# Kernel tuning notes

Hardware: AMD Instinct MI355X
Metric: run time of the kernel (lower is better)

Reference implementation:

```python
import jax, jax.numpy as jnp
import numpy as np

B, NQ, D, NH, L, P = 8, 1000, 256, 8, 4, 4
DFF = 1024
HD = D // NH
SHAPES = np.array([[128, 128], [64, 64], [32, 32], [16, 16]], dtype=np.int64)
S = int((SHAPES[:, 0] * SHAPES[:, 1]).sum())  # 21760
LEVEL_START = np.concatenate([np.zeros(1, np.int64), np.cumsum(SHAPES[:, 0] * SHAPES[:, 1])[:-1]])


def setup_inputs() -> dict:
    key = jax.random.key(0)
    ks = jax.random.split(key, 20)
    w = lambda k, shape, s=0.02: jax.random.normal(k, shape, jnp.float32) * s
    z = lambda n: jnp.zeros((n,), jnp.float32)
    return dict(
        query=w(ks[0], (B, NQ, D), 1.0),
        query_pos=w(ks[1], (B, NQ, D), 1.0),
        reference_points=jax.random.uniform(ks[2], (B, NQ, L, 4), jnp.float32),
        input_flatten=w(ks[3], (B, S, D), 1.0),
        input_spatial_shapes=SHAPES,
        input_level_start_index=LEVEL_START,
        Wq=w(ks[4], (D, D)), bq=z(D), Wk=w(ks[5], (D, D)), bk=z(D),
        Wv=w(ks[6], (D, D)), bv=z(D), Wo=w(ks[7], (D, D)), bo=z(D),
        ln1_g=jnp.ones((D,), jnp.float32), ln1_b=z(D),
        W_off=w(ks[8], (D, NH * L * P * 2)), b_off=z(NH * L * P * 2),
        W_attn=w(ks[9], (D, NH * L * P)), b_attn=z(NH * L * P),
        W_val=w(ks[10], (D, D)), b_val=z(D),
        W_cout=w(ks[11], (D, D)), b_cout=z(D),
        ln2_g=jnp.ones((D,), jnp.float32), ln2_b=z(D),
        W1=w(ks[12], (D, DFF)), b1=z(DFF),
        W2=w(ks[13], (DFF, D)), b2=z(D),
        ln3_g=jnp.ones((D,), jnp.float32), ln3_b=z(D),
    )


def layer_norm(x, g, b, eps=1e-5):
    mu = x.mean(-1, keepdims=True)
    var = ((x - mu) ** 2).mean(-1, keepdims=True)
    return (x - mu) / jnp.sqrt(var + eps) * g + b


def _ms_deform(value, shapes_np, loc, aw):
    # value: (B,S,NH,HD); loc: (B,Nq,NH,L,P,2) in [0,1]; aw: (B,Nq,NH,L,P)
    Bz, _, nh, hd = value.shape
    Nq = loc.shape[1]
    awt = aw.transpose(0, 2, 1, 3, 4)  # (B,NH,Nq,L,P)
    acc = jnp.zeros((Bz, nh, Nq, hd), value.dtype)
    start = 0
    for lvl in range(shapes_np.shape[0]):
        Hl, Wl = int(shapes_np[lvl, 0]), int(shapes_np[lvl, 1])
        vf = value[:, start:start + Hl * Wl].transpose(0, 2, 1, 3)  # (B,NH,Hl*Wl,HD)
        start += Hl * Wl
        # grid_sample align_corners=False: pixel coord = loc * size - 0.5
        lx = loc[:, :, :, lvl, :, 0].transpose(0, 2, 1, 3) * Wl - 0.5  # (B,NH,Nq,P)
        ly = loc[:, :, :, lvl, :, 1].transpose(0, 2, 1, 3) * Hl - 0.5
        x0 = jnp.floor(lx); y0 = jnp.floor(ly)
        tx = lx - x0; ty = ly - y0
        x0i = x0.astype(jnp.int32); y0i = y0.astype(jnp.int32)

        def gather(xi, yi):
            valid = (xi >= 0) & (xi < Wl) & (yi >= 0) & (yi < Hl)
            idx = jnp.clip(yi, 0, Hl - 1) * Wl + jnp.clip(xi, 0, Wl - 1)
            out = jnp.take_along_axis(vf, idx.reshape(Bz, nh, Nq * P)[..., None], axis=2)
            return out.reshape(Bz, nh, Nq, P, hd) * valid[..., None]

        g00 = gather(x0i, y0i)
        g01 = gather(x0i + 1, y0i)
        g10 = gather(x0i, y0i + 1)
        g11 = gather(x0i + 1, y0i + 1)
        samp = (g00 * ((1 - tx) * (1 - ty))[..., None] + g01 * (tx * (1 - ty))[..., None]
                + g10 * ((1 - tx) * ty)[..., None] + g11 * (tx * ty)[..., None])  # (B,NH,Nq,P,HD)
        acc = acc + jnp.einsum('bhqp,bhqpd->bhqd', awt[:, :, :, lvl], samp)
    return acc.transpose(0, 2, 1, 3).reshape(Bz, Nq, nh * hd)


def reference(query, query_pos, reference_points, input_flatten, input_spatial_shapes,
              input_level_start_index, Wq, bq, Wk, bk, Wv, bv, Wo, bo, ln1_g, ln1_b,
              W_off, b_off, W_attn, b_attn, W_val, b_val, W_cout, b_cout, ln2_g, ln2_b,
              W1, b1, W2, b2, ln3_g, ln3_b):
    Bz, Nq, Dm = query.shape
    # --- self-attention (post-norm), pos added to Q/K only ---
    qp = query + query_pos
    q = (qp @ Wq + bq).reshape(Bz, Nq, NH, HD)
    k = (qp @ Wk + bk).reshape(Bz, Nq, NH, HD)
    v = (query @ Wv + bv).reshape(Bz, Nq, NH, HD)
    att = jax.nn.softmax(jnp.einsum('bqhd,bkhd->bhqk', q, k) / jnp.sqrt(jnp.float32(HD)), axis=-1)
    sa = jnp.einsum('bhqk,bkhd->bqhd', att, v).reshape(Bz, Nq, Dm) @ Wo + bo
    x = layer_norm(query + sa, ln1_g, ln1_b)
    # --- deformable cross-attention ---
    q2 = x + query_pos
    value = (input_flatten @ W_val + b_val).reshape(Bz, -1, NH, HD)
    off = (q2 @ W_off + b_off).reshape(Bz, Nq, NH, L, P, 2)
    aw = jax.nn.softmax((q2 @ W_attn + b_attn).reshape(Bz, Nq, NH, L * P), axis=-1)
    aw = aw.reshape(Bz, Nq, NH, L, P)
    rp = reference_points  # (B,Nq,L,4) cxcywh
    loc = rp[:, :, None, :, None, :2] + off / P * rp[:, :, None, :, None, 2:] * 0.5
    shapes_np = np.asarray(input_spatial_shapes)
    ca = _ms_deform(value, shapes_np, loc, aw) @ W_cout + b_cout
    x = layer_norm(x + ca, ln2_g, ln2_b)
    # --- FFN ---
    ffn = jax.nn.relu(x @ W1 + b1) @ W2 + b2
    return layer_norm(x + ffn, ln3_g, ln3_b)
```

## Files before the change

kernel.cpp:

```cpp
#include <hip/hip_runtime.h>
#include <hip/hip_bf16.h>

#define B_   8
#define NQ_  1000
#define D_   256
#define NH_  8
#define L_   4
#define P_   4
#define DFF_ 1024
#define HD_  32
#define S_   21760
#define NTOK (B_*NQ_)

typedef short  bf16x8 __attribute__((ext_vector_type(8)));
typedef float  f32x4  __attribute__((ext_vector_type(4)));

#define WAITBAR(N) asm volatile("s_waitcnt vmcnt(" #N ") lgkmcnt(0)\n\ts_barrier" ::: "memory")
#define ENDBAR()   asm volatile("s_barrier" ::: "memory")

__device__ inline unsigned short f32_to_bf16_bits(float f) {
    unsigned int u = __float_as_uint(f);
    unsigned int rounding = 0x7FFFu + ((u >> 16) & 1u);
    u += rounding;
    return (unsigned short)(u >> 16);
}
__device__ inline float bf16_bits_to_f32(unsigned short b) {
    return __uint_as_float(((unsigned int)b) << 16);
}
__device__ inline unsigned int pack_trunc(float f0, float f1) {
    return __builtin_amdgcn_perm(__float_as_uint(f1), __float_as_uint(f0), 0x07060302u);
}
__device__ inline void async_copy16(const void* g, void* l) {
    __builtin_amdgcn_global_load_lds((const __attribute__((address_space(1))) unsigned int*)g,
                                     (__attribute__((address_space(3))) unsigned int*)l, 16, 0, 0);
}

struct PrepArgs {
    const float* wsrc[10];
    unsigned short* wdst[10];
    int wK[10], wN[10];
    const float* bq; const float* bk; const float* boff; const float* battn;
    float* qkb; float* oab;
    const float* query; const float* qpos;
    unsigned short* q_bf; unsigned short* qp_bf;
};
__global__ __launch_bounds__(256) void prep_k(PrepArgs P)
{
    const int bid = blockIdx.x, tid = threadIdx.x;
    if (bid < 640) {
        const int job = bid >> 6, tile = bid & 63;
        const int K = P.wK[job], N = P.wN[job];
        const int tilesN = N >> 6;
        if (tile >= (K >> 6) * tilesN) return;
        const int kt = tile / tilesN, nt = tile - kt * tilesN;
        const int k0 = kt * 64, n0 = nt * 64;
        __shared__ unsigned short t_[64][65];
        const float* src = P.wsrc[job];
        unsigned short* dst = P.wdst[job];
        const int cc = tid & 63, rr = tid >> 6;
        #pragma unroll
        for (int i = 0; i < 16; i++) {
            int k = i * 4 + rr;
            t_[k][cc] = f32_to_bf16_bits(src[(size_t)(k0 + k) * N + n0 + cc]);
        }
        __syncthreads();
        #pragma unroll
        for (int i = 0; i < 16; i++) {
            int n = i * 4 + rr;
            dst[(size_t)(n0 + n) * K + k0 + cc] = t_[cc][n];
        }
    } else if (bid == 640) {
        P.qkb[tid]       = P.bq[tid];
        P.qkb[256 + tid] = P.bk[tid];
        P.oab[tid]       = P.boff[tid];
        if (tid < 128) P.oab[256 + tid] = P.battn[tid];
    } else {
        const int base = (bid - 641) * 1024 + tid;
        float4 fq[4][2], fp[4][2];
        #pragma unroll
        for (int i = 0; i < 4; i++) {
            const float* q = P.query + (size_t)(base + i * 256) * 8;
            const float* p = P.qpos  + (size_t)(base + i * 256) * 8;
            fq[i][0] = *reinterpret_cast<const float4*>(q);
            fq[i][1] = *reinterpret_cast<const float4*>(q + 4);
            fp[i][0] = *reinterpret_cast<const float4*>(p);
            fp[i][1] = *reinterpret_cast<const float4*>(p + 4);
        }
        #pragma unroll
        for (int i = 0; i < 4; i++) {
            uint4 tq, tp;
            tq.x = pack_trunc(fq[i][0].x, fq[i][0].y);
            tq.y = pack_trunc(fq[i][0].z, fq[i][0].w);
            tq.z = pack_trunc(fq[i][1].x, fq[i][1].y);
            tq.w = pack_trunc(fq[i][1].z, fq[i][1].w);
            tp.x = pack_trunc(fq[i][0].x + fp[i][0].x, fq[i][0].y + fp[i][0].y);
            tp.y = pack_trunc(fq[i][0].z + fp[i][0].z, fq[i][0].w + fp[i][0].w);
            tp.z = pack_trunc(fq[i][1].x + fp[i][1].x, fq[i][1].y + fp[i][1].y);
            tp.w = pack_trunc(fq[i][1].z + fp[i][1].z, fq[i][1].w + fp[i][1].w);
            *reinterpret_cast<uint4*>(P.q_bf  + (size_t)(base + i * 256) * 8) = tq;
            *reinterpret_cast<uint4*>(P.qp_bf + (size_t)(base + i * 256) * 8) = tp;
        }
    }
}

__global__ __launch_bounds__(256) void vgemmF(const float* __restrict__ Af,
                                              const unsigned short* __restrict__ Bt,
                                              const float* __restrict__ bias,
                                              unsigned short* __restrict__ Cb)
{
    constexpr int K = 256;
    constexpr int N = 256;
    __shared__ __align__(16) float          sA[2][128 * 32];
    __shared__ __align__(16) unsigned short sB[2][128 * 32];
    const int tid = threadIdx.x;
    const int w = tid >> 6, l = tid & 63;
    const int n0 = blockIdx.x * 128, m0 = blockIdx.y * 128;
    const int wr = w >> 1, wc = w & 1;
    const int lq = l & 15, g = l >> 4;

    f32x4 acc[4][4];
    #pragma unroll
    for (int i = 0; i < 4; i++)
        #pragma unroll
        for (int j = 0; j < 4; j++)
            #pragma unroll
            for (int r = 0; r < 4; r++) acc[i][j][r] = 0.f;

    auto issueA = [&](int t, int buf) {
        #pragma unroll
        for (int r = 0; r < 4; r++) {
            int lin = (r * 256 + tid) * 16;
            int row = lin >> 7;
            int kb  = (lin & 127) ^ ((row & 3) << 5);
            async_copy16(Af + (size_t)(m0 + row) * K + t * 32 + (kb >> 2),
                         (char*)sA[buf] + lin);
        }
    };
    auto issueB = [&](int t, int buf) {
        #pragma unroll
        for (int r = 0; r < 2; r++) {
            int lin = (r * 256 + tid) * 16;
            int row = lin >> 6;
            int kb  = (lin & 63) ^ ((row & 3) << 4);
            async_copy16(Bt + (size_t)(n0 + row) * K + t * 32 + (kb >> 1),
                         (char*)sB[buf] + lin);
        }
    };

    issueA(0, 0);
    issueB(0, 0);

    for (int t = 0; t < 8; t++) {
        const int cur = t & 1;
        if (t + 1 < 8) {
            issueA(t + 1, cur ^ 1);
            issueB(t + 1, cur ^ 1);
            WAITBAR(6);
        } else {
            WAITBAR(0);
        }

        bf16x8 afr[4], bfr[4];
        #pragma unroll
        for (int mi = 0; mi < 4; mi++) {
            int row = wr * 64 + mi * 16 + lq;
            int off = (g * 32) ^ ((row & 3) << 5);
            const char* p = (const char*)sA[cur] + row * 128 + off;
            float4 a0 = *reinterpret_cast<const float4*>(p);
            float4 a1 = *reinterpret_cast<const float4*>(p + 16);
            uint4 u;
            u.x = pack_trunc(a0.x, a0.y);
            u.y = pack_trunc(a0.z, a0.w);
            u.z = pack_trunc(a1.x, a1.y);
            u.w = pack_trunc(a1.z, a1.w);
            afr[mi] = *reinterpret_cast<bf16x8*>(&u);
        }
        #pragma unroll
        for (int ni = 0; ni < 4; ni++) {
            int row = wc * 64 + ni * 16 + lq;
            int off = (g * 16) ^ ((row & 3) << 4);
            bfr[ni] = *reinterpret_cast<const bf16x8*>((const char*)sB[cur] + row * 64 + off);
        }
        #pragma unroll
        for (int mi = 0; mi < 4; mi++)
            #pragma unroll
            for (int ni = 0; ni < 4; ni++)
                acc[mi][ni] = __builtin_amdgcn_mfma_f32_16x16x32_bf16(
                    afr[mi], bfr[ni], acc[mi][ni], 0, 0, 0);
        ENDBAR();
    }

    #pragma unroll
    for (int mi = 0; mi < 4; mi++) {
        #pragma unroll
        for (int ni = 0; ni < 4; ni++) {
            int col = n0 + wc * 64 + ni * 16 + lq;
            float bz = bias[col];
            #pragma unroll
            for (int rg = 0; rg < 4; rg++) {
                int row = m0 + wr * 64 + mi * 16 + g * 4 + rg;
                Cb[(size_t)row * N + col] = f32_to_bf16_bits(acc[mi][ni][rg] + bz);
            }
        }
    }
}

template<bool RELU, int CMODE, int BN, int K>
__global__ __launch_bounds__(256) void bgemm(const unsigned short* __restrict__ Ab,
                                             const unsigned short* __restrict__ Bt,
                                             const float* __restrict__ bias,
                                             float* __restrict__ Cf,
                                             unsigned short* __restrict__ Cb,
                                             int N)
{
    constexpr int NF   = BN / 16;
    constexpr int KF   = K / 32;
    constexpr int ROWB = K * 2;
    constexpr int FILL = BN * ROWB / 4096;

    __shared__ __align__(16) unsigned short sB[BN * K];

    const int tid = threadIdx.x;
    const int w = tid >> 6, l = tid & 63;
    const int g = l >> 4, lr = l & 15;
    const int n0 = blockIdx.x * BN;

    #pragma unroll
    for (int r = 0; r < FILL; r++) {
        int lin = (r * 256 + tid) * 16;
        int row = lin / ROWB;
        int kb  = (lin & (ROWB - 1)) ^ ((row & 7) << 4);
        async_copy16(Bt + (size_t)(n0 + row) * K + (kb >> 1), (char*)sB + lin);
    }
    asm volatile("s_waitcnt vmcnt(0)\n\ts_barrier" ::: "memory");

    float bz[NF];
    #pragma unroll
    for (int nf = 0; nf < NF; nf++) bz[nf] = bias[n0 + nf * 16 + lr];

    const int m0w = blockIdx.y * 64 + w * 16;
    const int arow = m0w + lr;

    f32x4 acc[NF];
    #pragma unroll
    for (int nf = 0; nf < NF; nf++)
        #pragma unroll
        for (int r = 0; r < 4; r++) acc[nf][r] = 0.f;

    #pragma unroll
    for (int kf = 0; kf < KF; kf++) {
        bf16x8 af = *reinterpret_cast<const bf16x8*>(Ab + (size_t)arow * K + kf * 32 + g * 8);
        #pragma unroll
        for (int nf = 0; nf < NF; nf++) {
            int brow = nf * 16 + lr;
            bf16x8 bf = *reinterpret_cast<const bf16x8*>(
                (const char*)sB + brow * ROWB + ((kf * 64 + g * 16) ^ ((brow & 7) << 4)));
            acc[nf] = __builtin_amdgcn_mfma_f32_16x16x32_bf16(af, bf, acc[nf], 0, 0, 0);
        }
    }

    #pragma unroll
    for (int nf = 0; nf < NF; nf++) {
        int col = n0 + nf * 16 + lr;
        if constexpr (CMODE == 2) {
            int row0 = m0w + g * 4;
            int bb = row0 / 1000;
            int key = row0 - bb * 1000;
            ushort4 q4;
            q4.x = f32_to_bf16_bits(acc[nf][0] + bz[nf]);
            q4.y = f32_to_bf16_bits(acc[nf][1] + bz[nf]);
            q4.z = f32_to_bf16_bits(acc[nf][2] + bz[nf]);
            q4.w = f32_to_bf16_bits(acc[nf][3] + bz[nf]);
            *reinterpret_cast<ushort4*>(Cb + (size_t)bb * 262144 + (size_t)col * 1024 + key) = q4;
        } else {
            #pragma unroll
            for (int rg = 0; rg < 4; rg++) {
                int row = m0w + g * 4 + rg;
                float v = acc[nf][rg] + bz[nf];
                if (RELU) v = fmaxf(v, 0.f);
                if constexpr (CMODE == 1)
                    Cb[(size_t)row * N + col] = f32_to_bf16_bits(v);
                else
                    Cf[(size_t)row * N + col] = v;
            }
        }
    }
}

__global__ __launch_bounds__(256) void fattn_k(const unsigned short* __restrict__ qk,
                                               const unsigned short* __restrict__ vt,
                                               unsigned short* __restrict__ sa)
{
    const int b = blockIdx.z, h = blockIdx.y;
    const int tid = threadIdx.x;
    const int w = tid >> 6, l = tid & 63;
    const int lq = l & 15, g = l >> 4;
    const int q0 = blockIdx.x * 64 + w * 16;

    __shared__ __align__(16) unsigned short Ks[2][128 * 32];
    __shared__ __align__(16) unsigned short Vs[2][32 * 128];
    __shared__ __align__(16) unsigned short Ps[4][16 * 128];

    int qrow = q0 + lq; if (qrow > NQ_ - 1) qrow = NQ_ - 1;
    const bf16x8 qfrag = *reinterpret_cast<const bf16x8*>(
        qk + ((size_t)(b * NQ_ + qrow)) * 512 + h * 32 + g * 8);

    f32x4 O0 = {0.f, 0.f, 0.f, 0.f}, O1 = {0.f, 0.f, 0.f, 0.f};
    float m = -1e30f, lsum = 0.f;
    const float scale = 0.17677669529663687f;

    const size_t kbase = (size_t)b * (NQ_ * 512) + 256 + h * 32;
    const size_t vbase = (size_t)b * 262144 + (size_t)(h * 32) * 1024;
    const int swz = (lq & 7) << 4;

    auto issueKV = [&](int kt, int buf) {
        #pragma unroll
        for (int r = 0; r < 2; r++) {
            int lin = (r * 256 + tid) * 16;
            int krow = lin >> 6;
            int kb = (lin & 63) ^ ((krow & 7) << 4);
            async_copy16(qk + kbase + (size_t)(kt * 128 + krow) * 512 + (kb >> 1),
                         (char*)Ks[buf] + lin);
            int d = lin >> 8;
            int vb = (lin & 255) ^ ((d & 7) << 4);
            async_copy16(vt + vbase + (size_t)d * 1024 + kt * 128 + (vb >> 1),
                         (char*)Vs[buf] + lin);
        }
    };

    issueKV(0, 0);

    for (int kt = 0; kt < 8; kt++) {
        const int k0 = kt * 128;
        const int cur = kt & 1;
        asm volatile("s_waitcnt vmcnt(0) lgkmcnt(0)\n\ts_barrier" ::: "memory");
        if (kt < 7) issueKV(kt + 1, cur ^ 1);

        const unsigned short* Kc = Ks[cur];
        const unsigned short* Vc = Vs[cur];

        float t[8][4];
        float tmax = -1e30f;
        const bool tail = (k0 + 128 > NQ_);
        #pragma unroll
        for (int ni = 0; ni < 8; ni++) {
            int row = ni * 16 + lq;
            bf16x8 kf = *reinterpret_cast<const bf16x8*>(
                (const char*)Kc + row * 64 + ((g * 16) ^ swz));
            f32x4 st = __builtin_amdgcn_mfma_f32_16x16x32_bf16(
                kf, qfrag, (f32x4){0.f, 0.f, 0.f, 0.f}, 0, 0, 0);
            #pragma unroll
            for (int rg = 0; rg < 4; rg++) {
                float tv = st[rg] * scale;
                if (tail) {
                    int key = k0 + ni * 16 + g * 4 + rg;
                    tv = (key < NQ_) ? tv : -1e30f;
                }
                t[ni][rg] = tv;
                tmax = fmaxf(tmax, tv);
            }
        }
        tmax = fmaxf(tmax, __shfl_xor(tmax, 16));
        tmax = fmaxf(tmax, __shfl_xor(tmax, 32));
        float mnew = fmaxf(m, tmax);
        float corr = __expf(m - mnew);
        m = mnew;

        float rs = 0.f;
        unsigned int pk[8][2];
        #pragma unroll
        for (int ni = 0; ni < 8; ni++) {
            float p0 = __expf(t[ni][0] - mnew);
            float p1 = __expf(t[ni][1] - mnew);
            float p2 = __expf(t[ni][2] - mnew);
            float p3 = __expf(t[ni][3] - mnew);
            rs += (p0 + p1) + (p2 + p3);
            pk[ni][0] = ((unsigned)f32_to_bf16_bits(p0)) | (((unsigned)f32_to_bf16_bits(p1)) << 16);
            pk[ni][1] = ((unsigned)f32_to_bf16_bits(p2)) | (((unsigned)f32_to_bf16_bits(p3)) << 16);
        }
        rs += __shfl_xor(rs, 16);
        rs += __shfl_xor(rs, 32);
        lsum = lsum * corr + rs;

        float c0 = __shfl(corr, g * 4 + 0);
        float c1 = __shfl(corr, g * 4 + 1);
        float c2 = __shfl(corr, g * 4 + 2);
        float c3 = __shfl(corr, g * 4 + 3);
        O0[0] *= c0; O0[1] *= c1; O0[2] *= c2; O0[3] *= c3;
        O1[0] *= c0; O1[1] *= c1; O1[2] *= c2; O1[3] *= c3;

        unsigned short* Pw = Ps[w];
        #pragma unroll
        for (int ni = 0; ni < 8; ni++) {
            int byteoff = lq * 256 + ((ni * 32 + g * 8) ^ swz);
            *reinterpret_cast<uint2*>((char*)Pw + byteoff) = make_uint2(pk[ni][0], pk[ni][1]);
        }

        #pragma unroll
        for (int c = 0; c < 4; c++) {
            int rb = (c * 64 + g * 16) ^ swz;
            bf16x8 pa = *reinterpret_cast<const bf16x8*>((const char*)Pw + lq * 256 + rb);
            bf16x8 v0 = *reinterpret_cast<const bf16x8*>((const char*)Vc + lq * 256 + rb);
            bf16x8 v1 = *reinterpret_cast<const bf16x8*>((const char*)Vc + (16 + lq) * 256 + rb);
            O0 = __builtin_amdgcn_mfma_f32_16x16x32_bf16(pa, v0, O0, 0, 0, 0);
            O1 = __builtin_amdgcn_mfma_f32_16x16x32_bf16(pa, v1, O1, 0, 0, 0);
        }
    }

    float linv = 1.f / lsum;
    float i0 = __shfl(linv, g * 4 + 0);
    float i1 = __shfl(linv, g * 4 + 1);
    float i2 = __shfl(linv, g * 4 + 2);
    float i3 = __shfl(linv, g * 4 + 3);
    float iv[4] = {i0, i1, i2, i3};
    #pragma unroll
    for (int rg = 0; rg < 4; rg++) {
        int qg = q0 + g * 4 + rg;
        if (qg < NQ_) {
            size_t obase = ((size_t)(b * NQ_ + qg)) * 256 + h * 32;
            sa[obase + lq]      = f32_to_bf16_bits(O0[rg] * iv[rg]);
            sa[obase + 16 + lq] = f32_to_bf16_bits(O1[rg] * iv[rg]);
        }
    }
}

template<int OM>
__global__ __launch_bounds__(256) void ln_k(const float* __restrict__ a,
                                            const float* __restrict__ bsum,
                                            const float* __restrict__ pos,
                                            const float* __restrict__ g,
                                            const float* __restrict__ be,
                                            float* __restrict__ out,
                                            unsigned short* __restrict__ outb)
{
    const int wave = threadIdx.x >> 6, lane = threadIdx.x & 63;
    const int row = blockIdx.x * 4 + wave;
    float4 xa = reinterpret_cast<const float4*>(a + (size_t)row * 256)[lane];
    float4 xb = reinterpret_cast<const float4*>(bsum + (size_t)row * 256)[lane];
    float4 x = {xa.x + xb.x, xa.y + xb.y, xa.z + xb.z, xa.w + xb.w};
    float s  = x.x + x.y + x.z + x.w;
    float ss = x.x * x.x + x.y * x.y + x.z * x.z + x.w * x.w;
    #pragma unroll
    for (int off = 32; off > 0; off >>= 1) {
        s  += __shfl_xor(s, off);
        ss += __shfl_xor(ss, off);
    }
    float mu  = s * (1.f / 256.f);
    float var = ss * (1.f / 256.f) - mu * mu;
    float rstd = rsqrtf(var + 1e-5f);
    float4 gv = reinterpret_cast<const float4*>(g)[lane];
    float4 bv = reinterpret_cast<const float4*>(be)[lane];
    float4 o = {(x.x - mu) * rstd * gv.x + bv.x,
                (x.y - mu) * rstd * gv.y + bv.y,
                (x.z - mu) * rstd * gv.z + bv.z,
                (x.w - mu) * rstd * gv.w + bv.w};
    reinterpret_cast<float4*>(out + (size_t)row * 256)[lane] = o;
    if constexpr (OM == 1) {
        ushort4 q4;
        q4.x = f32_to_bf16_bits(o.x); q4.y = f32_to_bf16_bits(o.y);
        q4.z = f32_to_bf16_bits(o.z); q4.w = f32_to_bf16_bits(o.w);
        *reinterpret_cast<ushort4*>(outb + (size_t)row * 256 + lane * 4) = q4;
    } else if constexpr (OM == 2) {
        float4 pv = reinterpret_cast<const float4*>(pos + (size_t)row * 256)[lane];
        ushort4 q4;
        q4.x = f32_to_bf16_bits(o.x + pv.x); q4.y = f32_to_bf16_bits(o.y + pv.y);
        q4.z = f32_to_bf16_bits(o.z + pv.z); q4.w = f32_to_bf16_bits(o.w + pv.w);
        *reinterpret_cast<ushort4*>(outb + (size_t)row * 256 + lane * 4) = q4;
    }
}

__device__ inline unsigned int samp2(const unsigned short* __restrict__ v,
                                     int b, int st, int Wl, int Hl,
                                     int x, int y, int hc)
{
    bool valid = (x >= 0) & (x < Wl) & (y >= 0) & (y < Hl);
    int xc = min(max(x, 0), Wl - 1);
    int yc = min(max(y, 0), Hl - 1);
    size_t idx = ((size_t)(b * S_ + st + yc * Wl + xc)) * 256 + hc;
    unsigned int val = *reinterpret_cast<const unsigned int*>(v + idx);
    return valid ? val : 0u;
}

__global__ __launch_bounds__(256) void deform_k(const float* __restrict__ rp,
                                                const float* __restrict__ oa,
                                                const unsigned short* __restrict__ value,
                                                unsigned short* __restrict__ ca)
{
    const int tk = threadIdx.x >> 7;
    const int tok = blockIdx.x * 2 + tk;
    const int b = tok / NQ_;
    const int h = (threadIdx.x >> 4) & 7;
    const int cp = threadIdx.x & 15;
    const int hc = h * 32 + cp * 2;

    const float* awp = oa + (size_t)tok * 384 + 256 + h * 16;
    float w[16];
    float mx = -1e30f;
    #pragma unroll
    for (int i = 0; i < 16; i++) { w[i] = awp[i]; mx = fmaxf(mx, w[i]); }
    float sum = 0.f;
    #pragma unroll
    for (int i = 0; i < 16; i++) { w[i] = __expf(w[i] - mx); sum += w[i]; }
    const float inv = 1.f / sum;

    const float* rpp  = rp + (size_t)tok * (L_ * 4);
    const float* offp = oa + (size_t)tok * 384 + h * 32;

    const int lvlW[4] = {128, 64, 32, 16};
    const int lvlS[4] = {0, 16384, 20480, 21504};

    float acc0 = 0.f, acc1 = 0.f;
    #pragma unroll
    for (int l = 0; l < 4; l++) {
        const int Wl = lvlW[l], Hl = lvlW[l], st = lvlS[l];
        const float cx = rpp[l * 4 + 0], cy = rpp[l * 4 + 1];
        const float cw = rpp[l * 4 + 2], chh = rpp[l * 4 + 3];
        #pragma unroll
        for (int p = 0; p < 4; p++) {
            float ox = offp[l * 8 + p * 2 + 0];
            float oy = offp[l * 8 + p * 2 + 1];
            float lx = (cx + ox * 0.25f * cw * 0.5f) * Wl - 0.5f;
            float ly = (cy + oy * 0.25f * chh * 0.5f) * Hl - 0.5f;
            float x0f = floorf(lx), y0f = floorf(ly);
            float tx = lx - x0f, ty = ly - y0f;
            int x0 = (int)x0f, y0 = (int)y0f;
            unsigned int u00 = samp2(value, b, st, Wl, Hl, x0,     y0,     hc);
            unsigned int u01 = samp2(value, b, st, Wl, Hl, x0 + 1, y0,     hc);
            unsigned int u10 = samp2(value, b, st, Wl, Hl, x0,     y0 + 1, hc);
            unsigned int u11 = samp2(value, b, st, Wl, Hl, x0 + 1, y0 + 1, hc);
            float w00 = (1.f - tx) * (1.f - ty), w01 = tx * (1.f - ty);
            float w10 = (1.f - tx) * ty,         w11 = tx * ty;
            float g0 = bf16_bits_to_f32((unsigned short)u00) * w00
                     + bf16_bits_to_f32((unsigned short)u01) * w01
                     + bf16_bits_to_f32((unsigned short)u10) * w10
                     + bf16_bits_to_f32((unsigned short)u11) * w11;
            float g1 = bf16_bits_to_f32((unsigned short)(u00 >> 16)) * w00
                     + bf16_bits_to_f32((unsigned short)(u01 >> 16)) * w01
                     + bf16_bits_to_f32((unsigned short)(u10 >> 16)) * w10
                     + bf16_bits_to_f32((unsigned short)(u11 >> 16)) * w11;
            float wa = w[l * 4 + p] * inv;
            acc0 += wa * g0;
            acc1 += wa * g1;
        }
    }
    unsigned int packed = ((unsigned)f32_to_bf16_bits(acc0)) | (((unsigned)f32_to_bf16_bits(acc1)) << 16);
    *reinterpret_cast<unsigned int*>(ca + (size_t)tok * 256 + hc) = packed;
}

extern "C" void kernel_launch(void* const* d_in, const int* in_sizes, int n_in,
                              void* d_out, int out_size, void* d_ws, size_t ws_size,
                              hipStream_t stream)
{
    const float* query      = (const float*)d_in[0];
    const float* query_pos  = (const float*)d_in[1];
    const float* ref_pts    = (const float*)d_in[2];
    const float* input_flat = (const float*)d_in[3];
    const float* Wq = (const float*)d_in[6];  const float* bq = (const float*)d_in[7];
    const float* Wk = (const float*)d_in[8];  const float* bk = (const float*)d_in[9];
    const float* Wv = (const float*)d_in[10]; const float* bv = (const float*)d_in[11];
    const float* Wo = (const float*)d_in[12]; const float* bo = (const float*)d_in[13];
    const float* ln1g = (const float*)d_in[14]; const float* ln1b = (const float*)d_in[15];
    const float* W_off = (const float*)d_in[16]; const float* b_off = (const float*)d_in[17];
    const float* W_attn = (const float*)d_in[18]; const float* b_attn = (const float*)d_in[19];
    const float* W_val = (const float*)d_in[20]; const float* b_val = (const float*)d_in[21];
    const float* W_cout = (const float*)d_in[22]; const float* b_cout = (const float*)d_in[23];
    const float* ln2g = (const float*)d_in[24]; const float* ln2b = (const float*)d_in[25];
    const float* W1 = (const float*)d_in[26]; const float* b1 = (const float*)d_in[27];
    const float* W2 = (const float*)d_in[28]; const float* b2 = (const float*)d_in[29];
    const float* ln3g = (const float*)d_in[30]; const float* ln3b = (const float*)d_in[31];
    float* out = (float*)d_out;

    char* base = (char*)d_ws;
    size_t off = 0;
    auto alloc = [&](size_t bytes) { void* p = base + off; off += (bytes + 255) & ~(size_t)255; return p; };
    unsigned short* value_bf = (unsigned short*)alloc((size_t)B_ * S_ * 256 * 2);
    unsigned short* qk_bf = (unsigned short*)alloc((size_t)NTOK * 1024 * 2);
    unsigned short* h_bf = qk_bf;
    unsigned short* vt = (unsigned short*)alloc((size_t)B_ * 256 * 1024 * 2);
    float* oa_buf = (float*)alloc((size_t)NTOK * 384 * 4);
    float* tmp0   = (float*)alloc((size_t)NTOK * 256 * 4);
    float* x1     = (float*)alloc((size_t)NTOK * 256 * 4);
    float* x2     = (float*)alloc((size_t)NTOK * 256 * 4);
    unsigned short* sc_bf  = (unsigned short*)alloc((size_t)NTOK * 256 * 2);
    unsigned short* q_bf   = (unsigned short*)alloc((size_t)NTOK * 256 * 2);
    unsigned short* qp_bf  = (unsigned short*)alloc((size_t)NTOK * 256 * 2);
    unsigned short* x1p_bf = (unsigned short*)alloc((size_t)NTOK * 256 * 2);
    unsigned short* x2_bf  = (unsigned short*)alloc((size_t)NTOK * 256 * 2);
    unsigned short* wqk   = (unsigned short*)alloc(512 * 256 * 2);
    unsigned short* wv    = (unsigned short*)alloc(256 * 256 * 2);
    unsigned short* wo    = (unsigned short*)alloc(256 * 256 * 2);
    unsigned short* woa   = (unsigned short*)alloc(384 * 256 * 2);
    unsigned short* wval  = (unsigned short*)alloc(256 * 256 * 2);
    unsigned short* wcout = (unsigned short*)alloc(256 * 256 * 2);
    unsigned short* w1t   = (unsigned short*)alloc(1024 * 256 * 2);
    unsigned short* w2t   = (unsigned short*)alloc(256 * 1024 * 2);
    float* qkbias = (float*)alloc(512 * 4);
    float* oabias = (float*)alloc(384 * 4);

    dim3 blk(256);

    PrepArgs P;
    P.wsrc[0] = Wq;    P.wdst[0] = wqk;               P.wK[0] = 256;  P.wN[0] = 256;
    P.wsrc[1] = Wk;    P.wdst[1] = wqk + 256 * 256;   P.wK[1] = 256;  P.wN[1] = 256;
    P.wsrc[2] = Wv;    P.wdst[2] = wv;                P.wK[2] = 256;  P.wN[2] = 256;
    P.wsrc[3] = Wo;    P.wdst[3] = wo;                P.wK[3] = 256;  P.wN[3] = 256;
    P.wsrc[4] = W_off; P.wdst[4] = woa;               P.wK[4] = 256;  P.wN[4] = 256;
    P.wsrc[5] = W_attn;P.wdst[5] = woa + 256 * 256;   P.wK[5] = 256;  P.wN[5] = 128;
    P.wsrc[6] = W_val; P.wdst[6] = wval;              P.wK[6] = 256;  P.wN[6] = 256;
    P.wsrc[7] = W_cout;P.wdst[7] = wcout;             P.wK[7] = 256;  P.wN[7] = 256;
    P.wsrc[8] = W1;    P.wdst[8] = w1t;               P.wK[8] = 256;  P.wN[8] = 1024;
    P.wsrc[9] = W2;    P.wdst[9] = w2t;               P.wK[9] = 1024; P.wN[9] = 256;
    P.bq = bq; P.bk = bk; P.boff = b_off; P.battn = b_attn;
    P.qkb = qkbias; P.oab = oabias;
    P.query = query; P.qpos = query_pos; P.q_bf = q_bf; P.qp_bf = qp_bf;
    prep_k<<<891, blk, 0, stream>>>(P);

    bgemm<false, 1,  64, 256><<<dim3(8, 125), blk, 0, stream>>>(qp_bf, wqk, qkbias, nullptr, qk_bf, 512);
    bgemm<false, 2,  64, 256><<<dim3(4, 125), blk, 0, stream>>>(q_bf,  wv,  bv,     nullptr, vt,    256);
    fattn_k<<<dim3(16, NH_, B_), blk, 0, stream>>>(qk_bf, vt, sc_bf);
    bgemm<false, 0,  64, 256><<<dim3(4, 125), blk, 0, stream>>>(sc_bf, wo, bo, tmp0, nullptr, 256);
    ln_k<2><<<NTOK / 4, blk, 0, stream>>>(query, tmp0, query_pos, ln1g, ln1b, x1, x1p_bf);

    vgemmF<<<dim3(2, 1360), blk, 0, stream>>>(input_flat, wval, b_val, value_bf);
    bgemm<false, 0,  64, 256><<<dim3(6, 125), blk, 0, stream>>>(x1p_bf, woa, oabias, oa_buf, nullptr, 384);
    deform_k<<<NTOK / 2, blk, 0, stream>>>(ref_pts, oa_buf, value_bf, sc_bf);
    bgemm<false, 0,  64, 256><<<dim3(4, 125), blk, 0, stream>>>(sc_bf, wcout, b_cout, tmp0, nullptr, 256);
    ln_k<1><<<NTOK / 4, blk, 0, stream>>>(x1, tmp0, nullptr, ln2g, ln2b, x2, x2_bf);

    bgemm<true,  1,  64, 256><<<dim3(16, 125), blk, 0, stream>>>(x2_bf, w1t, b1, nullptr, h_bf, 1024);
    bgemm<false, 0,  32, 1024><<<dim3(8, 125), blk, 0, stream>>>(h_bf, w2t, b2, tmp0, nullptr, 256);
    ln_k<0><<<NTOK / 4, blk, 0, stream>>>(x2, tmp0, nullptr, ln3g, ln3b, out, nullptr);
}
```

Baseline: 253.7 us.

## Register-prefetch value GEMM with bf16 LDS tiles and 4-buffer ring

The value-projection GEMM stops using async global-to-LDS copies of fp32 A tiles. Each thread now loads A and B into registers three K-steps ahead, converts A to bf16 before writing it to swizzled LDS, and cycles through a 4-deep LDS ring so only one barrier per step is needed. This halves LDS traffic and footprint for A, removes the per-fragment conversion from the MFMA loop, and drops the trailing barrier. The cost is higher register pressure from 18 float4 prefetch registers per thread and reliance on the ring depth to avoid write-after-read hazards.

```diff
diff --git a/kernel.cpp b/kernel.cpp
--- a/kernel.cpp
+++ b/kernel.cpp
@@ -16,7 +16,7 @@
 typedef float  f32x4  __attribute__((ext_vector_type(4)));
 
 #define WAITBAR(N) asm volatile("s_waitcnt vmcnt(" #N ") lgkmcnt(0)\n\ts_barrier" ::: "memory")
-#define ENDBAR()   asm volatile("s_barrier" ::: "memory")
+#define LBAR()     asm volatile("s_waitcnt lgkmcnt(0)\n\ts_barrier" ::: "memory")
 
 __device__ inline unsigned short f32_to_bf16_bits(float f) {
     unsigned int u = __float_as_uint(f);
@@ -103,21 +103,57 @@
     }
 }
 
-__global__ __launch_bounds__(256) void vgemmF(const float* __restrict__ Af,
+__global__ __launch_bounds__(256) void vgemmP(const float* __restrict__ Af,
                                               const unsigned short* __restrict__ Bt,
                                               const float* __restrict__ bias,
                                               unsigned short* __restrict__ Cb)
 {
     constexpr int K = 256;
     constexpr int N = 256;
-    __shared__ __align__(16) float          sA[2][128 * 32];
-    __shared__ __align__(16) unsigned short sB[2][128 * 32];
+    __shared__ __align__(16) unsigned short sA[4][128 * 32];
+    __shared__ __align__(16) unsigned short sB[4][128 * 32];
+
     const int tid = threadIdx.x;
     const int w = tid >> 6, l = tid & 63;
     const int n0 = blockIdx.x * 128, m0 = blockIdx.y * 128;
     const int wr = w >> 1, wc = w & 1;
     const int lq = l & 15, g = l >> 4;
 
+    const int ldr = tid >> 1;
+    const int ldh = tid & 1;
+    const float*          aSrc = Af + (size_t)(m0 + ldr) * K + ldh * 16;
+    const unsigned short* bSrc = Bt + (size_t)(n0 + ldr) * K + ldh * 16;
+    const int wswz = ((ldr & 3) << 4);
+    const int o0 = (ldh * 32)      ^ wswz;
+    const int o1 = (ldh * 32 + 16) ^ wswz;
+
+    float4 fA[3][4];
+    float4 fB[3][2];
+
+    auto loadStage = [&](int t, int s) {
+        const float4* ap = reinterpret_cast<const float4*>(aSrc + t * 32);
+        fA[s][0] = ap[0]; fA[s][1] = ap[1]; fA[s][2] = ap[2]; fA[s][3] = ap[3];
+        const float4* bp = reinterpret_cast<const float4*>(bSrc + t * 32);
+        fB[s][0] = bp[0]; fB[s][1] = bp[1];
+    };
+    auto writeStage = [&](int s, int buf) {
+        uint4 c0, c1;
+        c0.x = pack_trunc(fA[s][0].x, fA[s][0].y);
+        c0.y = pack_trunc(fA[s][0].z, fA[s][0].w);
+        c0.z = pack_trunc(fA[s][1].x, fA[s][1].y);
+        c0.w = pack_trunc(fA[s][1].z, fA[s][1].w);
+        c1.x = pack_trunc(fA[s][2].x, fA[s][2].y);
+        c1.y = pack_trunc(fA[s][2].z, fA[s][2].w);
+        c1.z = pack_trunc(fA[s][3].x, fA[s][3].y);
+        c1.w = pack_trunc(fA[s][3].z, fA[s][3].w);
+        char* abase = (char*)sA[buf] + ldr * 64;
+        *reinterpret_cast<uint4*>(abase + o0) = c0;
+        *reinterpret_cast<uint4*>(abase + o1) = c1;
+        char* bbase = (char*)sB[buf] + ldr * 64;
+        *reinterpret_cast<float4*>(bbase + o0) = fB[s][0];
+        *reinterpret_cast<float4*>(bbase + o1) = fB[s][1];
+    };
+
     f32x4 acc[4][4];
     #pragma unroll
     for (int i = 0; i < 4; i++)
@@ -126,60 +162,30 @@
             #pragma unroll
             for (int r = 0; r < 4; r++) acc[i][j][r] = 0.f;
 
-    auto issueA = [&](int t, int buf) {
-        #pragma unroll
-        for (int r = 0; r < 4; r++) {
-            int lin = (r * 256 + tid) * 16;
-            int row = lin >> 7;
-            int kb  = (lin & 127) ^ ((row & 3) << 5);
-            async_copy16(Af + (size_t)(m0 + row) * K + t * 32 + (kb >> 2),
-                         (char*)sA[buf] + lin);
-        }
-    };
-    auto issueB = [&](int t, int buf) {
-        #pragma unroll
-        for (int r = 0; r < 2; r++) {
-            int lin = (r * 256 + tid) * 16;
-            int row = lin >> 6;
-            int kb  = (lin & 63) ^ ((row & 3) << 4);
-            async_copy16(Bt + (size_t)(n0 + row) * K + t * 32 + (kb >> 1),
-                         (char*)sB[buf] + lin);
-        }
-    };
-
-    issueA(0, 0);
-    issueB(0, 0);
-
+    loadStage(0, 0);
+    loadStage(1, 1);
+    loadStage(2, 2);
+
+    #pragma unroll
     for (int t = 0; t < 8; t++) {
-        const int cur = t & 1;
-        if (t + 1 < 8) {
-            issueA(t + 1, cur ^ 1);
-            issueB(t + 1, cur ^ 1);
-            WAITBAR(6);
-        } else {
-            WAITBAR(0);
-        }
+        const int s   = t % 3;
+        const int buf = t & 3;
+        writeStage(s, buf);
+        if (t + 3 < 8) loadStage(t + 3, s);
+        LBAR();
 
         bf16x8 afr[4], bfr[4];
         #pragma unroll
         for (int mi = 0; mi < 4; mi++) {
             int row = wr * 64 + mi * 16 + lq;
-            int off = (g * 32) ^ ((row & 3) << 5);
-            const char* p = (const char*)sA[cur] + row * 128 + off;
-            float4 a0 = *reinterpret_cast<const float4*>(p);
-            float4 a1 = *reinterpret_cast<const float4*>(p + 16);
-            uint4 u;
-            u.x = pack_trunc(a0.x, a0.y);
-            u.y = pack_trunc(a0.z, a0.w);
-            u.z = pack_trunc(a1.x, a1.y);
-            u.w = pack_trunc(a1.z, a1.w);
-            afr[mi] = *reinterpret_cast<bf16x8*>(&u);
+            int off = (g * 16) ^ ((row & 3) << 4);
+            afr[mi] = *reinterpret_cast<const bf16x8*>((const char*)sA[buf] + row * 64 + off);
         }
         #pragma unroll
         for (int ni = 0; ni < 4; ni++) {
             int row = wc * 64 + ni * 16 + lq;
             int off = (g * 16) ^ ((row & 3) << 4);
-            bfr[ni] = *reinterpret_cast<const bf16x8*>((const char*)sB[cur] + row * 64 + off);
+            bfr[ni] = *reinterpret_cast<const bf16x8*>((const char*)sB[buf] + row * 64 + off);
         }
         #pragma unroll
         for (int mi = 0; mi < 4; mi++)
@@ -187,7 +193,6 @@
             for (int ni = 0; ni < 4; ni++)
                 acc[mi][ni] = __builtin_amdgcn_mfma_f32_16x16x32_bf16(
                     afr[mi], bfr[ni], acc[mi][ni], 0, 0, 0);
-        ENDBAR();
     }
 
     #pragma unroll
@@ -621,7 +626,7 @@
     bgemm<false, 0,  64, 256><<<dim3(4, 125), blk, 0, stream>>>(sc_bf, wo, bo, tmp0, nullptr, 256);
     ln_k<2><<<NTOK / 4, blk, 0, stream>>>(query, tmp0, query_pos, ln1g, ln1b, x1, x1p_bf);
 
-    vgemmF<<<dim3(2, 1360), blk, 0, stream>>>(input_flat, wval, b_val, value_bf);
+    vgemmP<<<dim3(2, 1360), blk, 0, stream>>>(input_flat, wval, b_val, value_bf);
     bgemm<false, 0,  64, 256><<<dim3(6, 125), blk, 0, stream>>>(x1p_bf, woa, oabias, oa_buf, nullptr, 384);
     deform_k<<<NTOK / 2, blk, 0, stream>>>(ref_pts, oa_buf, value_bf, sc_bf);
     bgemm<false, 0,  64, 256><<<dim3(4, 125), blk, 0, stream>>>(sc_bf, wcout, b_cout, tmp0, nullptr, 256);
```

Measured after the change: 299.2 us. +17.9%, slower.
